# Kernel optimization log

Hardware: AMD Instinct MI355X
Metric: run time of the kernel (lower is better)

The kernel has to match this reference:

```python
import jax, jax.numpy as jnp
import numpy as np

D_MODEL = 256
N_HEADS = 8
N_LEVELS = 4
N_POINTS = 4
SHAPES = [(128, 128), (64, 64), (32, 32), (16, 16)]  # (H, W) per level


def _query_hw(Lq):
    h = int(Lq ** 0.5)
    w = Lq // h
    if h * w != Lq:
        facs = [(i, Lq // i) for i in range(1, int(Lq ** 0.5) + 1) if Lq % i == 0]
        h, w = min(facs, key=lambda t: abs(t[0] - t[1]))
    return h, w


def _grid_sample(img, grid):
    # img: [B, D, H, W]; grid: [B, Lq, P, 2] in [-1,1] (x, y)
    # bilinear, padding_mode='zeros', align_corners=False
    B, D, H, W = img.shape
    gx, gy = grid[..., 0], grid[..., 1]
    x = ((gx + 1.0) * W - 1.0) * 0.5
    y = ((gy + 1.0) * H - 1.0) * 0.5
    x0 = jnp.floor(x)
    y0 = jnp.floor(y)
    wx1 = x - x0
    wy1 = y - y0
    wx0 = 1.0 - wx1
    wy0 = 1.0 - wy1
    x0i = x0.astype(jnp.int32)
    y0i = y0.astype(jnp.int32)
    x1i = x0i + 1
    y1i = y0i + 1
    img_flat = img.reshape(B, D, H * W)

    def gather(yi, xi):
        valid = (xi >= 0) & (xi < W) & (yi >= 0) & (yi < H)
        idx = jnp.clip(yi, 0, H - 1) * W + jnp.clip(xi, 0, W - 1)  # [B,Lq,P]
        v = jnp.take_along_axis(img_flat, idx.reshape(B, 1, -1), axis=2)
        v = v.reshape(B, D, *yi.shape[1:])  # [B,D,Lq,P]
        return v * valid[:, None].astype(img.dtype)

    return (gather(y0i, x0i) * (wy0 * wx0)[:, None]
            + gather(y0i, x1i) * (wy0 * wx1)[:, None]
            + gather(y1i, x0i) * (wy1 * wx0)[:, None]
            + gather(y1i, x1i) * (wy1 * wx1)[:, None])


def _forward(query, input_flatten, spatial_shapes,
             W_off, b_off, W_attn, b_attn, W_val, b_val, W_out, b_out):
    N, Lq, C = query.shape
    M, L, P = N_HEADS, N_LEVELS, N_POINTS
    D = C // M
    shapes = np.asarray(spatial_shapes)  # static

    value = (input_flatten @ W_val + b_val).reshape(N, -1, M, D)
    off = (query @ W_off + b_off).reshape(N, Lq, M, L, P, 2)
    attn = jax.nn.softmax((query @ W_attn + b_attn).reshape(N, Lq, M, L * P), axis=-1)
    attn = attn.reshape(N, Lq, M, L, P)

    # normalized reference grid derived from Len_q (2D branch)
    qh, qw = _query_hw(Lq)
    ry, rx = jnp.meshgrid(jnp.linspace(0.5, qh - 0.5, qh) / qh,
                          jnp.linspace(0.5, qw - 0.5, qw) / qw, indexing='ij')
    ref = jnp.stack([rx.reshape(-1), ry.reshape(-1)], axis=-1)  # [Lq, 2] (x,y)
    norm = jnp.asarray(np.stack([shapes[:, 1], shapes[:, 0]], -1), jnp.float32)  # [L,2]=(W,H)
    loc = ref[None, :, None, None, None, :] + off / norm[None, None, None, :, None, :]
    grids = 2.0 * loc - 1.0  # [N,Lq,M,L,P,2]

    starts = np.concatenate([[0], np.cumsum(shapes[:, 0] * shapes[:, 1])])
    sampled = []
    for l in range(L):
        H, W = int(shapes[l, 0]), int(shapes[l, 1])
        v = value[:, starts[l]:starts[l + 1]]            # [N, H*W, M, D]
        v = v.transpose(0, 2, 3, 1).reshape(N * M, D, H, W)
        g = grids[:, :, :, l].transpose(0, 2, 1, 3, 4).reshape(N * M, Lq, P, 2)
        sampled.append(_grid_sample(v, g))               # [NM, D, Lq, P]

    vals = jnp.stack(sampled, axis=-2)                   # [NM, D, Lq, L, P]
    # faithful to original: values flattened (P, L)-major, weights (L, P)-major
    vals = vals.transpose(0, 1, 2, 4, 3).reshape(N * M, D, Lq, P * L)
    w = attn.transpose(0, 2, 1, 3, 4).reshape(N * M, 1, Lq, L * P)
    out = (vals * w).sum(-1).reshape(N, M * D, Lq).transpose(0, 2, 1)  # [N,Lq,C]
    return out @ W_out + b_out


def setup_inputs():
    key = jax.random.key(0)
    ks = jax.random.split(key, 12)
    N, Lq, C = 2, 16384, D_MODEL
    M, L, P = N_HEADS, N_LEVELS, N_POINTS
    Lin = sum(h * w for h, w in SHAPES)
    s = 0.02
    # sampling_offsets bias: original directional grid init
    thetas = np.arange(M, dtype=np.float32) * (2.0 * np.pi / M)
    gi = np.stack([np.cos(thetas), np.sin(thetas)], -1)
    gi = gi / np.abs(gi).max(-1, keepdims=True)
    gi = np.tile(gi.reshape(M, 1, 1, 2), (1, L, P, 1))
    for i in range(P):
        gi[:, :, i, :] *= (i + 1)
    inp = {
        'query': jax.random.normal(ks[0], (N, Lq, C), jnp.float32),
        'reference_points': jax.random.uniform(ks[1], (N, Lq, L, 2), jnp.float32),
        'input_flatten': jax.random.normal(ks[2], (N, Lin, C), jnp.float32),
        'spatial_shapes': jnp.array(SHAPES, jnp.int32),
        'level_start_index': jnp.array(np.concatenate([[0], np.cumsum([h * w for h, w in SHAPES[:-1]])]), jnp.int32),
        'W_off': jax.random.normal(ks[3], (C, M * L * P * 2), jnp.float32) * s,
        'b_off': jnp.asarray(gi.reshape(-1), jnp.float32),
        'W_attn': jax.random.normal(ks[4], (C, M * L * P), jnp.float32) * s,
        'b_attn': jnp.zeros((M * L * P,), jnp.float32),
        'W_val': jax.random.normal(ks[5], (C, C), jnp.float32) * (1.0 / np.sqrt(C)),
        'b_val': jnp.zeros((C,), jnp.float32),
        'W_out': jax.random.normal(ks[6], (C, C), jnp.float32) * (1.0 / np.sqrt(C)),
        'b_out': jnp.zeros((C,), jnp.float32),
    }
    return inp


def reference(query, reference_points, input_flatten, spatial_shapes, level_start_index,
              W_off, b_off, W_attn, b_attn, W_val, b_val, W_out, b_out):
    assert reference_points.shape[-1] == 2
    return _forward(query, input_flatten, spatial_shapes,
                    W_off, b_off, W_attn, b_attn, W_val, b_val, W_out, b_out)
```

## Files before the change

kernel.cpp:

```cpp
#include <hip/hip_runtime.h>
#include <math.h>

#define NB   2
#define LQ   16384
#define CDIM 256
#define MH   8
#define DH   32
#define LIN  21760
#define NPIX (NB * LIN)

typedef __attribute__((ext_vector_type(8))) _Float16 f16x8;
typedef __attribute__((ext_vector_type(4))) _Float16 f16x4;
typedef __attribute__((ext_vector_type(4))) float    f32x4;

__device__ __forceinline__ void async16(const void* g, void* l) {
    __builtin_amdgcn_global_load_lds(
        (const __attribute__((address_space(1))) void*)g,
        (__attribute__((address_space(3))) void*)l,
        16, 0, 0);
}

__device__ __forceinline__ int xcd_swizzle(int b, int nwg) {
    return (b & 7) * (nwg >> 3) + (b >> 3);
}

__global__ __launch_bounds__(256) void tsplit_all_kernel(
    const float* __restrict__ Wv, const float* __restrict__ Wo,
    const float* __restrict__ Wf, const float* __restrict__ Wa,
    _Float16* __restrict__ Wvt, _Float16* __restrict__ Wot, _Float16* __restrict__ Wct)
{
    const int i = blockIdx.x * 256 + threadIdx.x;
    const int r = i >> 8;
    const int kk = i & 255;
    if (r < 256) {
        Wvt[r * 256 + kk] = (_Float16)Wv[kk * 256 + r];
    } else if (r < 512) {
        const int n = r - 256;
        Wot[n * 256 + kk] = (_Float16)Wo[kk * 256 + n];
    } else if (r < 768) {
        const int n = r - 512;
        Wct[n * 256 + kk] = (_Float16)Wf[kk * 256 + n];
    } else {
        const int n = r - 768;
        Wct[(256 + n) * 256 + kk] = (_Float16)Wa[kk * 128 + n];
    }
}


__device__ __forceinline__ void stage_f16_half(
    const _Float16* __restrict__ Src, int brow0, int ph, _Float16* Dsh, int tid)
{
    #pragma unroll
    for (int j = 0; j < 8; ++j) {
        const int s = tid + 256 * j;
        const int row = s >> 4, ch = s & 15;
        const int cl = ch ^ (row & 7);
        async16(Src + (size_t)(brow0 + row) * 256 + ph * 128 + cl * 8, Dsh + s * 8);
    }
}

__device__ __forceinline__ void mfma_phase(
    const _Float16* Ash, const _Float16* Bsh, int wave, int quad, int l16,
    f32x4 (&acc)[2][8])
{
    #pragma unroll
    for (int t = 0; t < 4; ++t) {
        f16x8 ah[2];
        #pragma unroll
        for (int r = 0; r < 2; ++r) {
            const int arow = wave * 32 + r * 16 + l16;
            const int pa = (t * 4 + quad) ^ (arow & 7);
            ah[r] = *(const f16x8*)&Ash[arow * 128 + pa * 8];
        }
        #pragma unroll
        for (int half = 0; half < 2; ++half) {
            f16x8 bh[4];
            #pragma unroll
            for (int c = 0; c < 4; ++c) {
                const int brow = half * 64 + c * 16 + l16;
                const int pb = (t * 4 + quad) ^ (brow & 7);
                bh[c] = *(const f16x8*)&Bsh[brow * 128 + pb * 8];
            }
            #pragma unroll
            for (int r = 0; r < 2; ++r)
                #pragma unroll
                for (int c = 0; c < 4; ++c)
                    acc[r][half * 4 + c] = __builtin_amdgcn_mfma_f32_16x16x32_f16(
                        bh[c], ah[r], acc[r][half * 4 + c], 0, 0, 0);
        }
    }
}

__device__ __forceinline__ void core_f32_128(
    const float* __restrict__ A, const _Float16* __restrict__ Bt,
    int bm, int bn, _Float16* Ash, _Float16* Bsh, f32x4 (&acc)[2][8])
{
    const int tid = threadIdx.x;
    const int wave = tid >> 6, lane = tid & 63;
    const int quad = lane >> 4, l16 = lane & 15;
    #pragma unroll
    for (int ph = 0; ph < 2; ++ph) {
        if (ph) __syncthreads();
        float4 r0[8], r1[8];
        #pragma unroll
        for (int i = 0; i < 8; ++i) {
            const int v = tid + 256 * i;
            const int row = v >> 4, ch = v & 15;
            const float* src = A + (size_t)(bm + row) * 256 + ph * 128 + ch * 8;
            r0[i] = *(const float4*)src;
            r1[i] = *(const float4*)(src + 4);
        }
        stage_f16_half(Bt, bn, ph, Bsh, tid);
        #pragma unroll
        for (int i = 0; i < 8; ++i) {
            const int v = tid + 256 * i;
            const int row = v >> 4, ch = v & 15;
            f16x8 h;
            h[0] = (_Float16)r0[i].x; h[1] = (_Float16)r0[i].y;
            h[2] = (_Float16)r0[i].z; h[3] = (_Float16)r0[i].w;
            h[4] = (_Float16)r1[i].x; h[5] = (_Float16)r1[i].y;
            h[6] = (_Float16)r1[i].z; h[7] = (_Float16)r1[i].w;
            *(f16x8*)&Ash[row * 128 + ((ch ^ (row & 7)) * 8)] = h;
        }
        __syncthreads();
        mfma_phase(Ash, Bsh, wave, quad, l16, acc);
    }
}

__device__ __forceinline__ void core_f16_128(
    const _Float16* __restrict__ A, const _Float16* __restrict__ Bt,
    int bm, int bn, _Float16* Ash, _Float16* Bsh, f32x4 (&acc)[2][8])
{
    const int tid = threadIdx.x;
    const int wave = tid >> 6, lane = tid & 63;
    const int quad = lane >> 4, l16 = lane & 15;
    #pragma unroll
    for (int ph = 0; ph < 2; ++ph) {
        if (ph) __syncthreads();
        stage_f16_half(A, bm, ph, Ash, tid);
        stage_f16_half(Bt, bn, ph, Bsh, tid);
        __syncthreads();
        mfma_phase(Ash, Bsh, wave, quad, l16, acc);
    }
}

template <int OUT_MODE>
__device__ __forceinline__ void gemm_epilogue(
    f32x4 (&acc)[2][8], int bm, int bn, int wave, int quad, int l16,
    const float* bias0, const float* bias1, void* C0, void* C1, int N, int N0)
{
    void* Cb; const float* bb; int ldc, coff;
    if (bn < N0) { Cb = C0; bb = bias0; ldc = N0;     coff = 0;  }
    else         { Cb = C1; bb = bias1; ldc = N - N0; coff = N0; }
    #pragma unroll
    for (int cidx = 0; cidx < 8; ++cidx) {
        const int col = bn + cidx * 16 + quad * 4 - coff;
        const float4 bia = *(const float4*)&bb[col];
        #pragma unroll
        for (int r = 0; r < 2; ++r) {
            const int rr = bm + wave * 32 + r * 16 + l16;
            float4 v;
            v.x = acc[r][cidx][0] + bia.x;
            v.y = acc[r][cidx][1] + bia.y;
            v.z = acc[r][cidx][2] + bia.z;
            v.w = acc[r][cidx][3] + bia.w;
            if (OUT_MODE == 0) {
                *(float4*)&((float*)Cb)[(size_t)rr * ldc + col] = v;
            } else {
                f16x4 h;
                h[0] = (_Float16)v.x; h[1] = (_Float16)v.y;
                h[2] = (_Float16)v.z; h[3] = (_Float16)v.w;
                *(f16x4*)&((_Float16*)Cb)[((size_t)(col >> 5) * NPIX + rr) * 32 + (col & 31)] = h;
            }
        }
    }
}

__global__ __launch_bounds__(256) void gemm12_v3(
    const float* __restrict__ IF, const float* __restrict__ Q,
    const _Float16* __restrict__ Wvt, const _Float16* __restrict__ Wct,
    const float* __restrict__ b_val, const float* __restrict__ b_off,
    const float* __restrict__ b_attn,
    _Float16* __restrict__ value16, float* __restrict__ offbuf, float* __restrict__ attnbuf)
{
    __shared__ __align__(16) _Float16 Ash[128 * 128];
    __shared__ __align__(16) _Float16 Bsh[128 * 128];
    f32x4 acc[2][8] = {};
    const int tid = threadIdx.x;
    const int wave = tid >> 6, lane = tid & 63;
    const int quad = lane >> 4, l16 = lane & 15;
    const int wid = xcd_swizzle(blockIdx.x, 1448);

    if (wid < 680) {
        const int bm = (wid >> 1) * 128, bn = (wid & 1) * 128;
        core_f32_128(IF, Wvt, bm, bn, Ash, Bsh, acc);
        gemm_epilogue<2>(acc, bm, bn, wave, quad, l16,
                         b_val, b_val, value16, value16, 256, 256);
    } else {
        const int r = wid - 680;
        const int bm = (r / 3) * 128, bn = (r % 3) * 128;
        core_f32_128(Q, Wct, bm, bn, Ash, Bsh, acc);
        gemm_epilogue<0>(acc, bm, bn, wave, quad, l16,
                         b_off, b_attn, offbuf, attnbuf, 384, 256);
    }
}

__global__ __launch_bounds__(256) void gemm3_v3(
    const _Float16* __restrict__ A, const _Float16* __restrict__ Wot,
    const float* __restrict__ b_out, float* __restrict__ out)
{
    __shared__ __align__(16) _Float16 Ash[128 * 128];
    __shared__ __align__(16) _Float16 Bsh[128 * 128];
    f32x4 acc[2][8] = {};
    const int tid = threadIdx.x;
    const int wave = tid >> 6, lane = tid & 63;
    const int quad = lane >> 4, l16 = lane & 15;
    const int wid = xcd_swizzle(blockIdx.x, 512);
    const int bm = (wid >> 1) * 128, bn = (wid & 1) * 128;
    core_f16_128(A, Wot, bm, bn, Ash, Bsh, acc);
    gemm_epilogue<0>(acc, bm, bn, wave, quad, l16,
                     b_out, b_out, out, out, 256, 256);
}

__global__ __launch_bounds__(256) void sample_kernel_v10(
    const _Float16* __restrict__ value,
    const float* __restrict__ off,
    const float* __restrict__ attn,
    _Float16* __restrict__ outv)
{
    __shared__ __align__(16) int4   ivt[128][8];
    __shared__ __align__(16) float4 wvt[128][8];

    const int tid = threadIdx.x;
    const int qbase = blockIdx.x * 8;

    #pragma unroll
    for (int j = 0; j < 4; ++j) {
        const int t  = tid + 256 * j;
        const int q  = t >> 7;
        const int m  = (t >> 4) & 7;
        const int pt = t & 15;
        const int l  = pt >> 2;
        const int p  = pt & 3;
        const int qi = qbase + q;
        const int lq = qi & (LQ - 1);
        const int n  = qi >> 14;

        const int Hl = 128 >> l;
        const int STARTS[4] = {0, 16384, 20480, 21504};

        const float2 oxy = *(const float2*)&off[(size_t)qi * 256 + m * 32 + pt * 2];

        const float logit = attn[(size_t)qi * 128 + m * 16 + p * 4 + l];
        float mx = logit;
        #pragma unroll
        for (int d = 1; d < 16; d <<= 1) mx = fmaxf(mx, __shfl_xor(mx, d, 16));
        const float e = __expf(logit - mx);
        float sm = e;
        #pragma unroll
        for (int d = 1; d < 16; d <<= 1) sm += __shfl_xor(sm, d, 16);
        const float w = e / sm;

        const float refx = ((lq & 127) + 0.5f) * (1.0f / 128.0f);
        const float refy = ((lq >> 7)  + 0.5f) * (1.0f / 128.0f);

        const float x = refx * (float)Hl + oxy.x - 0.5f;
        const float y = refy * (float)Hl + oxy.y - 0.5f;
        const float x0f = floorf(x), y0f = floorf(y);
        const int x0 = (int)x0f, y0 = (int)y0f;
        const int x1 = x0 + 1,  y1 = y0 + 1;
        const float fx = x - x0f, fy = y - y0f;
        const float gx = 1.f - fx, gy = 1.f - fy;

        const float vx0 = (x0 >= 0 && x0 < Hl) ? 1.f : 0.f;
        const float vx1 = (x1 >= 0 && x1 < Hl) ? 1.f : 0.f;
        const float vy0 = (y0 >= 0 && y0 < Hl) ? 1.f : 0.f;
        const float vy1 = (y1 >= 0 && y1 < Hl) ? 1.f : 0.f;

        const int x0c = min(max(x0, 0), Hl - 1);
        const int x1c = min(max(x1, 0), Hl - 1);
        const int y0c = min(max(y0, 0), Hl - 1);
        const int y1c = min(max(y1, 0), Hl - 1);

        const int baseb = m * (NPIX * 64) + (n * LIN + STARTS[l]) * 64;
        const int i00 = baseb + (y0c * Hl + x0c) * 64;
        const int i01 = baseb + (y0c * Hl + x1c) * 64;
        const int i10 = baseb + (y1c * Hl + x0c) * 64;
        const int i11 = baseb + (y1c * Hl + x1c) * 64;

        float4 wv;
        wv.x = w * gy * gx * vy0 * vx0;
        wv.y = w * gy * fx * vy0 * vx1;
        wv.z = w * fy * gx * vy1 * vx0;
        wv.w = w * fy * fx * vy1 * vx1;

        const int cc = m ^ (pt & 7);
        int4 iv = {i00, i01, i10, i11};
        ivt[q * 16 + pt][cc] = iv;
        wvt[q * 16 + pt][cc] = wv;
    }
    __syncthreads();

    const int q  = tid >> 5;
    const int m  = (tid >> 2) & 7;
    const int d8 = tid & 3;
    const int qi = qbase + q;
    const unsigned dd = (unsigned)(d8 * 16);
    const char* vp = (const char*)value;

    f32x4 accL = {0.f, 0.f, 0.f, 0.f};
    f32x4 accH = {0.f, 0.f, 0.f, 0.f};
    #pragma unroll
    for (int pt = 0; pt < 16; ++pt) {
        const int cc = m ^ (pt & 7);
        const int4  iv = ivt[q * 16 + pt][cc];
        const float4 wv = wvt[q * 16 + pt][cc];
        const f16x8 v00 = *(const f16x8*)(vp + ((unsigned)iv.x + dd));
        const f16x8 v01 = *(const f16x8*)(vp + ((unsigned)iv.y + dd));
        const f16x8 v10 = *(const f16x8*)(vp + ((unsigned)iv.z + dd));
        const f16x8 v11 = *(const f16x8*)(vp + ((unsigned)iv.w + dd));
        f32x4 l00 = {(float)v00[0], (float)v00[1], (float)v00[2], (float)v00[3]};
        f32x4 h00 = {(float)v00[4], (float)v00[5], (float)v00[6], (float)v00[7]};
        f32x4 l01 = {(float)v01[0], (float)v01[1], (float)v01[2], (float)v01[3]};
        f32x4 h01 = {(float)v01[4], (float)v01[5], (float)v01[6], (float)v01[7]};
        f32x4 l10 = {(float)v10[0], (float)v10[1], (float)v10[2], (float)v10[3]};
        f32x4 h10 = {(float)v10[4], (float)v10[5], (float)v10[6], (float)v10[7]};
        f32x4 l11 = {(float)v11[0], (float)v11[1], (float)v11[2], (float)v11[3]};
        f32x4 h11 = {(float)v11[4], (float)v11[5], (float)v11[6], (float)v11[7]};
        accL += wv.x * l00 + wv.y * l01 + wv.z * l10 + wv.w * l11;
        accH += wv.x * h00 + wv.y * h01 + wv.z * h10 + wv.w * h11;
    }

    f16x8 o;
    o[0] = (_Float16)accL[0]; o[1] = (_Float16)accL[1];
    o[2] = (_Float16)accL[2]; o[3] = (_Float16)accL[3];
    o[4] = (_Float16)accH[0]; o[5] = (_Float16)accH[1];
    o[6] = (_Float16)accH[2]; o[7] = (_Float16)accH[3];
    *(f16x8*)&outv[(size_t)qi * 256 + m * 32 + d8 * 8] = o;
}

extern "C" void kernel_launch(void* const* d_in, const int* in_sizes, int n_in,
                              void* d_out, int out_size, void* d_ws, size_t ws_size,
                              hipStream_t stream)
{
    const float* query         = (const float*)d_in[0];
    const float* input_flatten = (const float*)d_in[2];
    const float* W_off  = (const float*)d_in[5];
    const float* b_off  = (const float*)d_in[6];
    const float* W_attn = (const float*)d_in[7];
    const float* b_attn = (const float*)d_in[8];
    const float* W_val  = (const float*)d_in[9];
    const float* b_val  = (const float*)d_in[10];
    const float* W_out  = (const float*)d_in[11];
    const float* b_out  = (const float*)d_in[12];
    float* out = (float*)d_out;

    char* w = (char*)d_ws;
    _Float16* Sf16 = (_Float16*)w;
    _Float16* value16 = (_Float16*)(w + 23068672);
    float*    attnbuf = (float*)(w + 67633152);
    _Float16* Wvt = (_Float16*)(w + 84410368);
    _Float16* Wot = Wvt + 65536;
    _Float16* Wct = Wot + 65536;
    float* offbuf = out;

    dim3 blk(256);

    tsplit_all_kernel<<<896, blk, 0, stream>>>(W_val, W_out, W_off, W_attn, Wvt, Wot, Wct);

    gemm12_v3<<<1448, blk, 0, stream>>>(
        input_flatten, query, Wvt, Wct, b_val, b_off, b_attn,
        value16, offbuf, attnbuf);

    sample_kernel_v10<<<4096, blk, 0, stream>>>(value16, offbuf, attnbuf, Sf16);

    gemm3_v3<<<512, blk, 0, stream>>>(Sf16, Wot, b_out, out);
}
```

Before: 225.3 us.

## Restructure GEMMs to full-width 64-row tiles streaming weights from global memory

Replaces the 128x128 tiled GEMMs, which staged both operands through LDS over two K phases, with 64-row blocks that cover the full output width. Only the activation tile (64x256, full K) goes to LDS with a single barrier, and weight fragments are read straight from global/L2 inside the MFMA loop. Each activation row is now read and converted once instead of once per N-tile, and LDS use drops, which may allow more blocks per CU. The cost is repeated global weight loads with no LDS reuse across waves, which could add latency, and more accumulator registers in the 384-wide query GEMM.

```diff
diff --git a/kernel.cpp b/kernel.cpp
--- a/kernel.cpp
+++ b/kernel.cpp
@@ -47,179 +47,137 @@
 }
 
 
-__device__ __forceinline__ void stage_f16_half(
-    const _Float16* __restrict__ Src, int brow0, int ph, _Float16* Dsh, int tid)
-{
+template <int NTW, bool A_F32>
+__device__ __forceinline__ void stream_core(
+    const void* __restrict__ Araw, const _Float16* __restrict__ Wt,
+    int bm, _Float16* Ash, f32x4 (&acc)[NTW][4])
+{
+    const int tid = threadIdx.x;
+    const int wave = tid >> 6, lane = tid & 63;
+    const int quad = lane >> 4, l16 = lane & 15;
+
+    if (A_F32) {
+        const float* A = (const float*)Araw;
+        float4 r0[8], r1[8];
+        #pragma unroll
+        for (int j = 0; j < 8; ++j) {
+            const int s = tid + 256 * j;
+            const int row = s >> 5, ch = s & 31;
+            const float* src = A + (size_t)(bm + row) * 256 + ch * 8;
+            r0[j] = *(const float4*)src;
+            r1[j] = *(const float4*)(src + 4);
+        }
+        #pragma unroll
+        for (int j = 0; j < 8; ++j) {
+            const int s = tid + 256 * j;
+            const int row = s >> 5, ch = s & 31;
+            f16x8 h;
+            h[0] = (_Float16)r0[j].x; h[1] = (_Float16)r0[j].y;
+            h[2] = (_Float16)r0[j].z; h[3] = (_Float16)r0[j].w;
+            h[4] = (_Float16)r1[j].x; h[5] = (_Float16)r1[j].y;
+            h[6] = (_Float16)r1[j].z; h[7] = (_Float16)r1[j].w;
+            *(f16x8*)&Ash[row * 256 + ((ch ^ (row & 7)) * 8)] = h;
+        }
+    } else {
+        const _Float16* A = (const _Float16*)Araw;
+        #pragma unroll
+        for (int j = 0; j < 8; ++j) {
+            const int s = tid + 256 * j;
+            const int row = s >> 5, ch = s & 31;
+            const int cl = ch ^ (row & 7);
+            async16(A + (size_t)(bm + row) * 256 + cl * 8, Ash + s * 8);
+        }
+    }
+    __syncthreads();
+
     #pragma unroll
-    for (int j = 0; j < 8; ++j) {
-        const int s = tid + 256 * j;
-        const int row = s >> 4, ch = s & 15;
-        const int cl = ch ^ (row & 7);
-        async16(Src + (size_t)(brow0 + row) * 256 + ph * 128 + cl * 8, Dsh + s * 8);
-    }
-}
-
-__device__ __forceinline__ void mfma_phase(
-    const _Float16* Ash, const _Float16* Bsh, int wave, int quad, int l16,
-    f32x4 (&acc)[2][8])
-{
-    #pragma unroll
-    for (int t = 0; t < 4; ++t) {
-        f16x8 ah[2];
-        #pragma unroll
-        for (int r = 0; r < 2; ++r) {
-            const int arow = wave * 32 + r * 16 + l16;
-            const int pa = (t * 4 + quad) ^ (arow & 7);
-            ah[r] = *(const f16x8*)&Ash[arow * 128 + pa * 8];
-        }
-        #pragma unroll
-        for (int half = 0; half < 2; ++half) {
-            f16x8 bh[4];
+    for (int k = 0; k < 8; ++k) {
+        f16x8 ah[4];
+        #pragma unroll
+        for (int rg = 0; rg < 4; ++rg) {
+            const int arow = rg * 16 + l16;
+            ah[rg] = *(const f16x8*)&Ash[arow * 256 + (((k * 4 + quad) ^ (arow & 7)) * 8)];
+        }
+        #pragma unroll
+        for (int ntw = 0; ntw < NTW; ++ntw) {
+            const int nt = ntw * 4 + wave;
+            const f16x8 bh = *(const f16x8*)&Wt[(size_t)(nt * 16 + l16) * 256 + k * 32 + quad * 8];
             #pragma unroll
-            for (int c = 0; c < 4; ++c) {
-                const int brow = half * 64 + c * 16 + l16;
-                const int pb = (t * 4 + quad) ^ (brow & 7);
-                bh[c] = *(const f16x8*)&Bsh[brow * 128 + pb * 8];
-            }
-            #pragma unroll
-            for (int r = 0; r < 2; ++r)
-                #pragma unroll
-                for (int c = 0; c < 4; ++c)
-                    acc[r][half * 4 + c] = __builtin_amdgcn_mfma_f32_16x16x32_f16(
-                        bh[c], ah[r], acc[r][half * 4 + c], 0, 0, 0);
-        }
-    }
-}
-
-__device__ __forceinline__ void core_f32_128(
-    const float* __restrict__ A, const _Float16* __restrict__ Bt,
-    int bm, int bn, _Float16* Ash, _Float16* Bsh, f32x4 (&acc)[2][8])
+            for (int rg = 0; rg < 4; ++rg)
+                acc[ntw][rg] = __builtin_amdgcn_mfma_f32_16x16x32_f16(
+                    bh, ah[rg], acc[ntw][rg], 0, 0, 0);
+        }
+    }
+}
+
+template <int NTW, int OUT_MODE>
+__device__ __forceinline__ void stream_epi(
+    f32x4 (&acc)[NTW][4], int bm,
+    const float* __restrict__ bias0, const float* __restrict__ bias1,
+    void* __restrict__ C0, void* __restrict__ C1, int N, int N0)
 {
     const int tid = threadIdx.x;
     const int wave = tid >> 6, lane = tid & 63;
     const int quad = lane >> 4, l16 = lane & 15;
     #pragma unroll
-    for (int ph = 0; ph < 2; ++ph) {
-        if (ph) __syncthreads();
-        float4 r0[8], r1[8];
-        #pragma unroll
-        for (int i = 0; i < 8; ++i) {
-            const int v = tid + 256 * i;
-            const int row = v >> 4, ch = v & 15;
-            const float* src = A + (size_t)(bm + row) * 256 + ph * 128 + ch * 8;
-            r0[i] = *(const float4*)src;
-            r1[i] = *(const float4*)(src + 4);
-        }
-        stage_f16_half(Bt, bn, ph, Bsh, tid);
-        #pragma unroll
-        for (int i = 0; i < 8; ++i) {
-            const int v = tid + 256 * i;
-            const int row = v >> 4, ch = v & 15;
-            f16x8 h;
-            h[0] = (_Float16)r0[i].x; h[1] = (_Float16)r0[i].y;
-            h[2] = (_Float16)r0[i].z; h[3] = (_Float16)r0[i].w;
-            h[4] = (_Float16)r1[i].x; h[5] = (_Float16)r1[i].y;
-            h[6] = (_Float16)r1[i].z; h[7] = (_Float16)r1[i].w;
-            *(f16x8*)&Ash[row * 128 + ((ch ^ (row & 7)) * 8)] = h;
-        }
-        __syncthreads();
-        mfma_phase(Ash, Bsh, wave, quad, l16, acc);
-    }
-}
-
-__device__ __forceinline__ void core_f16_128(
-    const _Float16* __restrict__ A, const _Float16* __restrict__ Bt,
-    int bm, int bn, _Float16* Ash, _Float16* Bsh, f32x4 (&acc)[2][8])
-{
-    const int tid = threadIdx.x;
-    const int wave = tid >> 6, lane = tid & 63;
-    const int quad = lane >> 4, l16 = lane & 15;
-    #pragma unroll
-    for (int ph = 0; ph < 2; ++ph) {
-        if (ph) __syncthreads();
-        stage_f16_half(A, bm, ph, Ash, tid);
-        stage_f16_half(Bt, bn, ph, Bsh, tid);
-        __syncthreads();
-        mfma_phase(Ash, Bsh, wave, quad, l16, acc);
-    }
-}
-
-template <int OUT_MODE>
-__device__ __forceinline__ void gemm_epilogue(
-    f32x4 (&acc)[2][8], int bm, int bn, int wave, int quad, int l16,
-    const float* bias0, const float* bias1, void* C0, void* C1, int N, int N0)
-{
-    void* Cb; const float* bb; int ldc, coff;
-    if (bn < N0) { Cb = C0; bb = bias0; ldc = N0;     coff = 0;  }
-    else         { Cb = C1; bb = bias1; ldc = N - N0; coff = N0; }
-    #pragma unroll
-    for (int cidx = 0; cidx < 8; ++cidx) {
-        const int col = bn + cidx * 16 + quad * 4 - coff;
-        const float4 bia = *(const float4*)&bb[col];
-        #pragma unroll
-        for (int r = 0; r < 2; ++r) {
-            const int rr = bm + wave * 32 + r * 16 + l16;
+    for (int ntw = 0; ntw < NTW; ++ntw) {
+        const int nt = ntw * 4 + wave;
+        const int col = nt * 16 + quad * 4;
+        const bool first = col < N0;
+        void* Cb        = first ? C0 : C1;
+        const float* bb = first ? bias0 : bias1;
+        const int ldc   = first ? N0 : (N - N0);
+        const int c2    = first ? col : col - N0;
+        const float4 bia = *(const float4*)&bb[c2];
+        #pragma unroll
+        for (int rg = 0; rg < 4; ++rg) {
+            const int rr = bm + rg * 16 + l16;
             float4 v;
-            v.x = acc[r][cidx][0] + bia.x;
-            v.y = acc[r][cidx][1] + bia.y;
-            v.z = acc[r][cidx][2] + bia.z;
-            v.w = acc[r][cidx][3] + bia.w;
+            v.x = acc[ntw][rg][0] + bia.x;
+            v.y = acc[ntw][rg][1] + bia.y;
+            v.z = acc[ntw][rg][2] + bia.z;
+            v.w = acc[ntw][rg][3] + bia.w;
             if (OUT_MODE == 0) {
-                *(float4*)&((float*)Cb)[(size_t)rr * ldc + col] = v;
+                *(float4*)&((float*)Cb)[(size_t)rr * ldc + c2] = v;
             } else {
                 f16x4 h;
                 h[0] = (_Float16)v.x; h[1] = (_Float16)v.y;
                 h[2] = (_Float16)v.z; h[3] = (_Float16)v.w;
-                *(f16x4*)&((_Float16*)Cb)[((size_t)(col >> 5) * NPIX + rr) * 32 + (col & 31)] = h;
+                *(f16x4*)&((_Float16*)Cb)[((size_t)(c2 >> 5) * NPIX + rr) * 32 + (c2 & 31)] = h;
             }
         }
     }
 }
 
-__global__ __launch_bounds__(256) void gemm12_v3(
+__global__ __launch_bounds__(256) void gemm12_v4(
     const float* __restrict__ IF, const float* __restrict__ Q,
     const _Float16* __restrict__ Wvt, const _Float16* __restrict__ Wct,
     const float* __restrict__ b_val, const float* __restrict__ b_off,
     const float* __restrict__ b_attn,
     _Float16* __restrict__ value16, float* __restrict__ offbuf, float* __restrict__ attnbuf)
 {
-    __shared__ __align__(16) _Float16 Ash[128 * 128];
-    __shared__ __align__(16) _Float16 Bsh[128 * 128];
-    f32x4 acc[2][8] = {};
-    const int tid = threadIdx.x;
-    const int wave = tid >> 6, lane = tid & 63;
-    const int quad = lane >> 4, l16 = lane & 15;
-    const int wid = xcd_swizzle(blockIdx.x, 1448);
-
+    __shared__ __align__(16) _Float16 Ash[64 * 256];
+    const int wid = xcd_swizzle(blockIdx.x, 1192);
     if (wid < 680) {
-        const int bm = (wid >> 1) * 128, bn = (wid & 1) * 128;
-        core_f32_128(IF, Wvt, bm, bn, Ash, Bsh, acc);
-        gemm_epilogue<2>(acc, bm, bn, wave, quad, l16,
-                         b_val, b_val, value16, value16, 256, 256);
+        f32x4 acc[4][4] = {};
+        stream_core<4, true>(IF, Wvt, wid * 64, Ash, acc);
+        stream_epi<4, 2>(acc, wid * 64, b_val, b_val, value16, value16, 256, 256);
     } else {
-        const int r = wid - 680;
-        const int bm = (r / 3) * 128, bn = (r % 3) * 128;
-        core_f32_128(Q, Wct, bm, bn, Ash, Bsh, acc);
-        gemm_epilogue<0>(acc, bm, bn, wave, quad, l16,
-                         b_off, b_attn, offbuf, attnbuf, 384, 256);
-    }
-}
-
-__global__ __launch_bounds__(256) void gemm3_v3(
+        f32x4 acc[6][4] = {};
+        stream_core<6, true>(Q, Wct, (wid - 680) * 64, Ash, acc);
+        stream_epi<6, 0>(acc, (wid - 680) * 64, b_off, b_attn, offbuf, attnbuf, 384, 256);
+    }
+}
+
+__global__ __launch_bounds__(256) void gemm3_v4(
     const _Float16* __restrict__ A, const _Float16* __restrict__ Wot,
     const float* __restrict__ b_out, float* __restrict__ out)
 {
-    __shared__ __align__(16) _Float16 Ash[128 * 128];
-    __shared__ __align__(16) _Float16 Bsh[128 * 128];
-    f32x4 acc[2][8] = {};
-    const int tid = threadIdx.x;
-    const int wave = tid >> 6, lane = tid & 63;
-    const int quad = lane >> 4, l16 = lane & 15;
+    __shared__ __align__(16) _Float16 Ash[64 * 256];
     const int wid = xcd_swizzle(blockIdx.x, 512);
-    const int bm = (wid >> 1) * 128, bn = (wid & 1) * 128;
-    core_f16_128(A, Wot, bm, bn, Ash, Bsh, acc);
-    gemm_epilogue<0>(acc, bm, bn, wave, quad, l16,
-                     b_out, b_out, out, out, 256, 256);
+    f32x4 acc[4][4] = {};
+    stream_core<4, false>(A, Wot, wid * 64, Ash, acc);
+    stream_epi<4, 0>(acc, wid * 64, b_out, b_out, out, out, 256, 256);
 }
 
 __global__ __launch_bounds__(256) void sample_kernel_v10(
@@ -368,11 +326,11 @@
 
     tsplit_all_kernel<<<896, blk, 0, stream>>>(W_val, W_out, W_off, W_attn, Wvt, Wot, Wct);
 
-    gemm12_v3<<<1448, blk, 0, stream>>>(
+    gemm12_v4<<<1192, blk, 0, stream>>>(
         input_flatten, query, Wvt, Wct, b_val, b_off, b_attn,
         value16, offbuf, attnbuf);
 
     sample_kernel_v10<<<4096, blk, 0, stream>>>(value16, offbuf, attnbuf, Sf16);
 
-    gemm3_v3<<<512, blk, 0, stream>>>(Sf16, Wot, b_out, out);
-}
+    gemm3_v4<<<512, blk, 0, stream>>>(Sf16, Wot, b_out, out);
+}
```

Measured after the change: 247.3 us. 1.1x slower.

## Double-buffer GEMM K-loop in 64-wide chunks to overlap loads with MFMA

Applied to the files above, without the earlier changes.

Both GEMM kernels now split K=256 into four 64-wide chunks with two LDS buffers each for A and B. The next chunk's global loads (async LDS loads for f16, register loads plus f16 conversion for f32 A) are issued before the MFMAs on the current chunk, so memory latency overlaps compute. LDS footprint stays at 64KB per block, but there are four barriers instead of two and more live registers for the prefetched A.

```diff
diff --git a/kernel.cpp b/kernel.cpp
--- a/kernel.cpp
+++ b/kernel.cpp
@@ -47,30 +47,51 @@
 }
 
 
-__device__ __forceinline__ void stage_f16_half(
-    const _Float16* __restrict__ Src, int brow0, int ph, _Float16* Dsh, int tid)
+__device__ __forceinline__ void stageB64(const _Float16* __restrict__ Bt, int brow0,
+                                         int k0, _Float16* Bsh, int tid)
+{
+    #pragma unroll
+    for (int j = 0; j < 4; ++j) {
+        const int s = tid + 256 * j;
+        const int row = s >> 3, ch = s & 7;
+        const int cl = ch ^ (row & 7);
+        async16(Bt + (size_t)(brow0 + row) * 256 + k0 + cl * 8, Bsh + s * 8);
+    }
+}
+
+__device__ __forceinline__ void issueA64(const float* __restrict__ A, int bm, int k0,
+                                         int tid, float4 (&ar)[8])
 {
     #pragma unroll
     for (int j = 0; j < 8; ++j) {
         const int s = tid + 256 * j;
-        const int row = s >> 4, ch = s & 15;
-        const int cl = ch ^ (row & 7);
-        async16(Src + (size_t)(brow0 + row) * 256 + ph * 128 + cl * 8, Dsh + s * 8);
-    }
-}
-
-__device__ __forceinline__ void mfma_phase(
-    const _Float16* Ash, const _Float16* Bsh, int wave, int quad, int l16,
-    f32x4 (&acc)[2][8])
-{
-    #pragma unroll
-    for (int t = 0; t < 4; ++t) {
+        const int row = s >> 4, c4 = s & 15;
+        ar[j] = *(const float4*)(A + (size_t)(bm + row) * 256 + k0 + c4 * 4);
+    }
+}
+__device__ __forceinline__ void writeA64(_Float16* Ash, int tid, const float4 (&ar)[8])
+{
+    #pragma unroll
+    for (int j = 0; j < 8; ++j) {
+        const int s = tid + 256 * j;
+        const int row = s >> 4, c4 = s & 15;
+        f16x4 h;
+        h[0] = (_Float16)ar[j].x; h[1] = (_Float16)ar[j].y;
+        h[2] = (_Float16)ar[j].z; h[3] = (_Float16)ar[j].w;
+        *(f16x4*)&Ash[row * 64 + ((c4 >> 1) ^ (row & 7)) * 8 + (c4 & 1) * 4] = h;
+    }
+}
+
+__device__ __forceinline__ void mfma64(const _Float16* Ash, const _Float16* Bsh,
+                                       int wave, int quad, int l16, f32x4 (&acc)[2][8])
+{
+    #pragma unroll
+    for (int kk = 0; kk < 2; ++kk) {
         f16x8 ah[2];
         #pragma unroll
         for (int r = 0; r < 2; ++r) {
             const int arow = wave * 32 + r * 16 + l16;
-            const int pa = (t * 4 + quad) ^ (arow & 7);
-            ah[r] = *(const f16x8*)&Ash[arow * 128 + pa * 8];
+            ah[r] = *(const f16x8*)&Ash[arow * 64 + (((kk * 4 + quad) ^ (arow & 7)) * 8)];
         }
         #pragma unroll
         for (int half = 0; half < 2; ++half) {
@@ -78,8 +99,7 @@
             #pragma unroll
             for (int c = 0; c < 4; ++c) {
                 const int brow = half * 64 + c * 16 + l16;
-                const int pb = (t * 4 + quad) ^ (brow & 7);
-                bh[c] = *(const f16x8*)&Bsh[brow * 128 + pb * 8];
+                bh[c] = *(const f16x8*)&Bsh[brow * 64 + (((kk * 4 + quad) ^ (brow & 7)) * 8)];
             }
             #pragma unroll
             for (int r = 0; r < 2; ++r)
@@ -91,56 +111,65 @@
     }
 }
 
-__device__ __forceinline__ void core_f32_128(
+__device__ __forceinline__ void core_f32_dbuf(
     const float* __restrict__ A, const _Float16* __restrict__ Bt,
-    int bm, int bn, _Float16* Ash, _Float16* Bsh, f32x4 (&acc)[2][8])
+    int bm, int bn, _Float16* Ash0, _Float16* Ash1, _Float16* Bsh0, _Float16* Bsh1,
+    f32x4 (&acc)[2][8])
 {
     const int tid = threadIdx.x;
     const int wave = tid >> 6, lane = tid & 63;
     const int quad = lane >> 4, l16 = lane & 15;
-    #pragma unroll
-    for (int ph = 0; ph < 2; ++ph) {
-        if (ph) __syncthreads();
-        float4 r0[8], r1[8];
-        #pragma unroll
-        for (int i = 0; i < 8; ++i) {
-            const int v = tid + 256 * i;
-            const int row = v >> 4, ch = v & 15;
-            const float* src = A + (size_t)(bm + row) * 256 + ph * 128 + ch * 8;
-            r0[i] = *(const float4*)src;
-            r1[i] = *(const float4*)(src + 4);
+
+    {
+        float4 ar[8];
+        issueA64(A, bm, 0, tid, ar);
+        stageB64(Bt, bn, 0, Bsh0, tid);
+        writeA64(Ash0, tid, ar);
+    }
+    __syncthreads();
+
+    #pragma unroll
+    for (int t = 0; t < 4; ++t) {
+        _Float16* AshC = (t & 1) ? Ash1 : Ash0;
+        _Float16* AshN = (t & 1) ? Ash0 : Ash1;
+        _Float16* BshC = (t & 1) ? Bsh1 : Bsh0;
+        _Float16* BshN = (t & 1) ? Bsh0 : Bsh1;
+        float4 ar[8];
+        if (t < 3) {
+            issueA64(A, bm, (t + 1) * 64, tid, ar);
+            stageB64(Bt, bn, (t + 1) * 64, BshN, tid);
         }
-        stage_f16_half(Bt, bn, ph, Bsh, tid);
-        #pragma unroll
-        for (int i = 0; i < 8; ++i) {
-            const int v = tid + 256 * i;
-            const int row = v >> 4, ch = v & 15;
-            f16x8 h;
-            h[0] = (_Float16)r0[i].x; h[1] = (_Float16)r0[i].y;
-            h[2] = (_Float16)r0[i].z; h[3] = (_Float16)r0[i].w;
-            h[4] = (_Float16)r1[i].x; h[5] = (_Float16)r1[i].y;
-            h[6] = (_Float16)r1[i].z; h[7] = (_Float16)r1[i].w;
-            *(f16x8*)&Ash[row * 128 + ((ch ^ (row & 7)) * 8)] = h;
-        }
+        mfma64(AshC, BshC, wave, quad, l16, acc);
+        if (t < 3) writeA64(AshN, tid, ar);
         __syncthreads();
-        mfma_phase(Ash, Bsh, wave, quad, l16, acc);
-    }
-}
-
-__device__ __forceinline__ void core_f16_128(
+    }
+}
+
+__device__ __forceinline__ void core_f16_dbuf(
     const _Float16* __restrict__ A, const _Float16* __restrict__ Bt,
-    int bm, int bn, _Float16* Ash, _Float16* Bsh, f32x4 (&acc)[2][8])
+    int bm, int bn, _Float16* Ash0, _Float16* Ash1, _Float16* Bsh0, _Float16* Bsh1,
+    f32x4 (&acc)[2][8])
 {
     const int tid = threadIdx.x;
     const int wave = tid >> 6, lane = tid & 63;
     const int quad = lane >> 4, l16 = lane & 15;
-    #pragma unroll
-    for (int ph = 0; ph < 2; ++ph) {
-        if (ph) __syncthreads();
-        stage_f16_half(A, bm, ph, Ash, tid);
-        stage_f16_half(Bt, bn, ph, Bsh, tid);
+
+    stageB64(A, bm, 0, Ash0, tid);
+    stageB64(Bt, bn, 0, Bsh0, tid);
+    __syncthreads();
+
+    #pragma unroll
+    for (int t = 0; t < 4; ++t) {
+        _Float16* AshC = (t & 1) ? Ash1 : Ash0;
+        _Float16* AshN = (t & 1) ? Ash0 : Ash1;
+        _Float16* BshC = (t & 1) ? Bsh1 : Bsh0;
+        _Float16* BshN = (t & 1) ? Bsh0 : Bsh1;
+        if (t < 3) {
+            stageB64(A, bm, (t + 1) * 64, AshN, tid);
+            stageB64(Bt, bn, (t + 1) * 64, BshN, tid);
+        }
+        mfma64(AshC, BshC, wave, quad, l16, acc);
         __syncthreads();
-        mfma_phase(Ash, Bsh, wave, quad, l16, acc);
     }
 }
 
@@ -176,15 +205,15 @@
     }
 }
 
-__global__ __launch_bounds__(256) void gemm12_v3(
+__global__ __launch_bounds__(256) void gemm12_v5(
     const float* __restrict__ IF, const float* __restrict__ Q,
     const _Float16* __restrict__ Wvt, const _Float16* __restrict__ Wct,
     const float* __restrict__ b_val, const float* __restrict__ b_off,
     const float* __restrict__ b_attn,
     _Float16* __restrict__ value16, float* __restrict__ offbuf, float* __restrict__ attnbuf)
 {
-    __shared__ __align__(16) _Float16 Ash[128 * 128];
-    __shared__ __align__(16) _Float16 Bsh[128 * 128];
+    __shared__ __align__(16) _Float16 Ash[2][128 * 64];
+    __shared__ __align__(16) _Float16 Bsh[2][128 * 64];
     f32x4 acc[2][8] = {};
     const int tid = threadIdx.x;
     const int wave = tid >> 6, lane = tid & 63;
@@ -193,31 +222,31 @@
 
     if (wid < 680) {
         const int bm = (wid >> 1) * 128, bn = (wid & 1) * 128;
-        core_f32_128(IF, Wvt, bm, bn, Ash, Bsh, acc);
+        core_f32_dbuf(IF, Wvt, bm, bn, Ash[0], Ash[1], Bsh[0], Bsh[1], acc);
         gemm_epilogue<2>(acc, bm, bn, wave, quad, l16,
                          b_val, b_val, value16, value16, 256, 256);
     } else {
         const int r = wid - 680;
         const int bm = (r / 3) * 128, bn = (r % 3) * 128;
-        core_f32_128(Q, Wct, bm, bn, Ash, Bsh, acc);
+        core_f32_dbuf(Q, Wct, bm, bn, Ash[0], Ash[1], Bsh[0], Bsh[1], acc);
         gemm_epilogue<0>(acc, bm, bn, wave, quad, l16,
                          b_off, b_attn, offbuf, attnbuf, 384, 256);
     }
 }
 
-__global__ __launch_bounds__(256) void gemm3_v3(
+__global__ __launch_bounds__(256) void gemm3_v5(
     const _Float16* __restrict__ A, const _Float16* __restrict__ Wot,
     const float* __restrict__ b_out, float* __restrict__ out)
 {
-    __shared__ __align__(16) _Float16 Ash[128 * 128];
-    __shared__ __align__(16) _Float16 Bsh[128 * 128];
+    __shared__ __align__(16) _Float16 Ash[2][128 * 64];
+    __shared__ __align__(16) _Float16 Bsh[2][128 * 64];
     f32x4 acc[2][8] = {};
     const int tid = threadIdx.x;
     const int wave = tid >> 6, lane = tid & 63;
     const int quad = lane >> 4, l16 = lane & 15;
     const int wid = xcd_swizzle(blockIdx.x, 512);
     const int bm = (wid >> 1) * 128, bn = (wid & 1) * 128;
-    core_f16_128(A, Wot, bm, bn, Ash, Bsh, acc);
+    core_f16_dbuf(A, Wot, bm, bn, Ash[0], Ash[1], Bsh[0], Bsh[1], acc);
     gemm_epilogue<0>(acc, bm, bn, wave, quad, l16,
                      b_out, b_out, out, out, 256, 256);
 }
@@ -368,11 +397,11 @@
 
     tsplit_all_kernel<<<896, blk, 0, stream>>>(W_val, W_out, W_off, W_attn, Wvt, Wot, Wct);
 
-    gemm12_v3<<<1448, blk, 0, stream>>>(
+    gemm12_v5<<<1448, blk, 0, stream>>>(
         input_flatten, query, Wvt, Wct, b_val, b_off, b_attn,
         value16, offbuf, attnbuf);
 
     sample_kernel_v10<<<4096, blk, 0, stream>>>(value16, offbuf, attnbuf, Sf16);
 
-    gemm3_v3<<<512, blk, 0, stream>>>(Sf16, Wot, b_out, out);
-}
+    gemm3_v5<<<512, blk, 0, stream>>>(Sf16, Wot, b_out, out);
+}
```

Result: slower. 231.8 us (+2.9%).
